# Kernel optimization log

Hardware: AMD Instinct MI355X
Metric: run time of the kernel (lower is better)

Reference implementation:

```python
import jax, jax.numpy as jnp
import numpy as np

# Static problem sizes (see shape_source)
B, D, H, W = 2, 16, 64, 64          # batch, sparse_shape = grid_size[::-1]
NV = 20000                           # active voxels per batch sample
CIN = 16                             # input_channels
THRESH = 0.5                         # FOCAL_THRESHOLD (used for kernel-offset mask)
EPS = 1e-3                           # BatchNorm eps from norm_fn
K_FORE = int(NV * THRESH)            # topk split: top int(N*threshold) voxels are foreground
# kernel_offsets: [[i,j,k] for i,j,k in (-1..1)^3] minus [0,0,0], applied to [z,y,x]
OFFSETS = [(i, j, k) for i in range(-1, 2) for j in range(-1, 2) for k in range(-1, 2) if (i, j, k) != (0, 0, 0)]


def _conv(x, w):
    # dense 3x3x3 conv == SubMConv3d math at active sites (inactive cells hold zeros)
    return jax.lax.conv_general_dilated(x, w, (1, 1, 1), 'SAME',
                                        dimension_numbers=('NDHWC', 'DHWIO', 'NDHWC'))


def _bn(x, g, b, m, v):
    # eval-mode BatchNorm1d over voxel features
    return (x - m) * (g * jax.lax.rsqrt(v + EPS)) + b


def setup_inputs() -> dict:
    rng = np.random.default_rng(0)
    coords = []
    for b in range(B):  # unique voxel coords per sample (spconv requires unique indices)
        lin = rng.permutation(D * H * W)[:NV]
        z = lin // (H * W); r = lin % (H * W)
        coords.append(np.stack([np.full(NV, b), z, r // W, r % W], 1))
    voxel_coords = jnp.asarray(np.concatenate(coords, 0), jnp.int32)  # [B*NV, 4] = [b,z,y,x]
    ks = jax.random.split(jax.random.key(0), 24)

    def bn_p(i, c):
        return (1.0 + 0.1 * jax.random.normal(ks[i], (c,)),
                0.1 * jax.random.normal(ks[i + 1], (c,)),
                0.1 * jax.random.normal(ks[i + 2], (c,)),
                jax.random.uniform(ks[i + 3], (c,), minval=0.5, maxval=1.5))

    g1, b1, m1, v1 = bn_p(4, 32)
    g2, b2, m2, v2 = bn_p(8, 64)
    g3, b3, m3, v3 = bn_p(12, 128)
    return dict(
        voxel_features=jax.random.normal(ks[0], (B * NV, CIN), jnp.float32),
        voxel_coords=voxel_coords,
        w1=0.08 * jax.random.normal(ks[1], (3, 3, 3, CIN, 32), jnp.float32),
        w2=0.06 * jax.random.normal(ks[2], (3, 3, 3, 32, 64), jnp.float32),
        w_imp=0.05 * jax.random.normal(ks[3], (3, 3, 3, 64, 27), jnp.float32),
        w_focal=0.04 * jax.random.normal(ks[16], (3, 3, 3, 64, 128), jnp.float32),
        g1=g1, b1=b1, m1=m1, v1=v1,
        g2=g2, b2=b2, m2=m2, v2=v2,
        g3=g3, b3=b3, m3=m3, v3=v3)


def reference(voxel_features, w1, g1, b1, m1, v1, w2, g2, b2, m2, v2,
              w_imp, w_focal, g3, b3, m3, v3, voxel_coords):
    bi, z, y, x = (voxel_coords[:, i] for i in range(4))
    # scatter sparse voxels into dense grid; zeros at inactive cells
    dense = jnp.zeros((B, D, H, W, CIN), voxel_features.dtype).at[bi, z, y, x].set(voxel_features)
    active = jnp.zeros((B, D, H, W), bool).at[bi, z, y, x].set(True)
    am = active[..., None].astype(voxel_features.dtype)

    # conv_input: two SubMConv3d + BN + ReLU (re-mask so inactive cells stay zero)
    h = jax.nn.relu(_bn(_conv(dense, w1), g1, b1, m1, v1)) * am   # -> 32
    h = jax.nn.relu(_bn(_conv(h, w2), g2, b2, m2, v2)) * am       # -> 64

    # conv_imp -> 27 logits; last = voxel importance, first 26 = kernel-offset importances
    imp = _conv(h, w_imp)
    mask_voxel = jax.nn.sigmoid(imp[..., -1])
    mask_kernel = jax.nn.sigmoid(imp[..., :26])

    # split_voxels with topk=True: foreground = top int(NV*thr) voxels per batch by importance
    mv_flat = jnp.where(active, mask_voxel, -jnp.inf).reshape(B, -1)
    kth = jax.lax.top_k(mv_flat, K_FORE)[0][:, -1]
    fore = active & (mask_voxel >= kth[:, None, None, None])

    # dilate foreground by kernel offsets where offset importance >= threshold.
    # New voxels carry zero features; check_repeat (index_add dedup) then reduces to:
    # final features == original features, final actives == active OR dilated candidates.
    new_act = active
    for i, (oz, oy, ox) in enumerate(OFFSETS):
        src = fore & (mask_kernel[..., i] >= THRESH)
        p = jnp.pad(src, ((0, 0), (1, 1), (1, 1), (1, 1)))  # zero(False)-pad for shift
        sh = p[:, 1 - oz:1 - oz + D, 1 - oy:1 - oy + H, 1 - ox:1 - ox + W]
        # original bound check is strict (>0), so plane 0 of each axis is invalid
        sh = sh.at[:, 0].set(False).at[:, :, 0].set(False).at[:, :, :, 0].set(False)
        new_act = new_act | sh

    # conv_focal on merged sparse set (new voxels have zero features -> dense conv matches)
    out = jax.nn.relu(_bn(_conv(h, w_focal), g3, b3, m3, v3)) * new_act[..., None].astype(h.dtype)
    return out  # densified encoded_spconv_tensor features [B, D, H, W, 128]
```

## Files before the change

kernel.cpp:

```cpp
#include <hip/hip_runtime.h>
#include <stdint.h>

#define Dd 16
#define Hh 64
#define Ww 64
#define NACT 40000
#define NVb 20000
#define KFORE 10000
#define EPSf 0.001f

typedef __attribute__((ext_vector_type(8))) short short8;
typedef __attribute__((ext_vector_type(4))) float f32x4;
typedef __attribute__((ext_vector_type(4))) unsigned short us4;

static __device__ __forceinline__ uint32_t f2sort(float f) {
    uint32_t u = __float_as_uint(f);
    return (u & 0x80000000u) ? ~u : (u | 0x80000000u);
}

static __device__ __forceinline__ unsigned short f2b(float f) {
    uint32_t u = __float_as_uint(f);
    return (unsigned short)((u + 0x7FFFu + ((u >> 16) & 1u)) >> 16);
}

static __device__ __forceinline__ int xcd_swz(int orig, int nwg) {
    int xcd = orig & 7, idx = orig >> 3;
    int q = nwg >> 3, r = nwg & 7;
    int base = xcd < r ? xcd * (q + 1) : r * (q + 1) + (xcd - r) * q;
    return base + idx;
}

__global__ void __launch_bounds__(256) k_scatter(const float* __restrict__ feat,
                                                 const int* __restrict__ coords,
                                                 float* __restrict__ dense16,
                                                 uint8_t* __restrict__ active,
                                                 uint8_t* __restrict__ new_act) {
    int i = blockIdx.x * 256 + threadIdx.x;
    if (i >= NACT) return;
    int b = coords[i * 4 + 0], z = coords[i * 4 + 1], y = coords[i * 4 + 2], x = coords[i * 4 + 3];
    int pos = ((b * Dd + z) * Hh + y) * Ww + x;
    active[pos] = 1;
    new_act[pos] = 1;
    const float4* f4 = (const float4*)(feat + (size_t)i * 16);
    float4* d4 = (float4*)(dense16 + (size_t)pos * 16);
    d4[0] = f4[0]; d4[1] = f4[1]; d4[2] = f4[2]; d4[3] = f4[3];
}

__global__ void __launch_bounds__(256) k_cnt(const uint8_t* __restrict__ mask,
                                             int* __restrict__ bcnt) {
    __shared__ int s[256];
    const int i = blockIdx.x * 256 + threadIdx.x;
    s[threadIdx.x] = mask[i] ? 1 : 0;
    __syncthreads();
    for (int off = 128; off > 0; off >>= 1) {
        if (threadIdx.x < off) s[threadIdx.x] += s[threadIdx.x + off];
        __syncthreads();
    }
    if (threadIdx.x == 0) bcnt[blockIdx.x] = s[0];
}

__global__ void __launch_bounds__(512) k_scan(const int* __restrict__ bcnt,
                                              int* __restrict__ boff, int* __restrict__ count) {
    __shared__ int s[512];
    const int t = threadIdx.x;
    const int v0 = bcnt[t];
    s[t] = v0;
    __syncthreads();
    for (int off = 1; off < 512; off <<= 1) {
        int v = s[t];
        if (t >= off) v += s[t - off];
        __syncthreads();
        s[t] = v;
        __syncthreads();
    }
    boff[t] = s[t] - v0;
    if (t == 511) *count = s[511];
}

__global__ void __launch_bounds__(256) k_emit(const uint8_t* __restrict__ mask,
                                              const int* __restrict__ boff,
                                              int* __restrict__ list) {
    __shared__ int s[256];
    const int i = blockIdx.x * 256 + threadIdx.x;
    const int pred = mask[i] ? 1 : 0;
    s[threadIdx.x] = pred;
    __syncthreads();
    for (int off = 1; off < 256; off <<= 1) {
        int v = s[threadIdx.x];
        if (threadIdx.x >= off) v += s[threadIdx.x - off];
        __syncthreads();
        s[threadIdx.x] = v;
        __syncthreads();
    }
    if (pred) list[boff[blockIdx.x] + s[threadIdx.x] - 1] = i;
}

__global__ void __launch_bounds__(256) k_conv1p(const int* __restrict__ list,
        const float* __restrict__ dense16, const float* __restrict__ w1,
        float* __restrict__ pbuf) {
    const int gb = xcd_swz(blockIdx.x, 157 * 3);
    const int chunk = gb / 3, tp = gb % 3;
    const int i = chunk * 256 + threadIdx.x;
    if (i >= NACT) return;
    const int pos = list[i];
    const int z = (pos >> 12) & 15, y = (pos >> 6) & 63, x = pos & 63;
    float acc[32];
    #pragma unroll
    for (int c = 0; c < 32; ++c) acc[c] = 0.f;
    const int dz = tp - 1;
    if ((unsigned)(z + dz) < Dd) {
        for (int tt = 0; tt < 9; ++tt) {
            const int dy = tt / 3 - 1, dx = tt % 3 - 1;
            if (!((unsigned)(y + dy) < Hh && (unsigned)(x + dx) < Ww)) continue;
            const float* row = dense16 + (size_t)(pos + dz * 4096 + dy * 64 + dx) * 16;
            const float* wt = w1 + (tp * 9 + tt) * 512;
            #pragma unroll
            for (int k4 = 0; k4 < 4; ++k4) {
                float4 xv = *(const float4*)(row + k4 * 4);
                float xs[4] = {xv.x, xv.y, xv.z, xv.w};
                #pragma unroll
                for (int j = 0; j < 4; ++j)
                    #pragma unroll
                    for (int c = 0; c < 32; ++c)
                        acc[c] = fmaf(xs[j], wt[(k4 * 4 + j) * 32 + c], acc[c]);
            }
        }
    }
    #pragma unroll
    for (int c = 0; c < 32; ++c) pbuf[(size_t)(tp * 32 + c) * NACT + i] = acc[c];
}

__global__ void __launch_bounds__(256) k_conv1c(const int* __restrict__ list,
        const float* __restrict__ pbuf,
        const float* __restrict__ g, const float* __restrict__ bta,
        const float* __restrict__ mu, const float* __restrict__ va,
        float* __restrict__ h1) {
    const int i = blockIdx.x * 256 + threadIdx.x;
    if (i >= NACT) return;
    const int pos = list[i];
    float res[32];
    #pragma unroll
    for (int c = 0; c < 32; ++c) {
        float s = pbuf[(size_t)c * NACT + i]
                + pbuf[(size_t)(32 + c) * NACT + i]
                + pbuf[(size_t)(64 + c) * NACT + i];
        const float sc = g[c] * (1.0f / sqrtf(va[c] + EPSf));
        res[c] = fmaxf(0.f, fmaf(s - mu[c], sc, bta[c]));
    }
    #pragma unroll
    for (int c4 = 0; c4 < 8; ++c4)
        *(float4*)(h1 + (size_t)pos * 32 + c4 * 4) = *(float4*)&res[c4 * 4];
}

__global__ void __launch_bounds__(256) k_conv2p(const int* __restrict__ list,
        const float* __restrict__ h1, const float* __restrict__ w2,
        float* __restrict__ pbuf) {
    const int gb = xcd_swz(blockIdx.x, 157 * 6);
    const int chunk = gb / 6, p = gb % 6;
    const int tp = p >> 1, cb = (p & 1) * 32;
    const int i = chunk * 256 + threadIdx.x;
    if (i >= NACT) return;
    const int pos = list[i];
    const int z = (pos >> 12) & 15, y = (pos >> 6) & 63, x = pos & 63;
    float acc[32];
    #pragma unroll
    for (int c = 0; c < 32; ++c) acc[c] = 0.f;
    const int dz = tp - 1;
    if ((unsigned)(z + dz) < Dd) {
        for (int tt = 0; tt < 9; ++tt) {
            const int dy = tt / 3 - 1, dx = tt % 3 - 1;
            if (!((unsigned)(y + dy) < Hh && (unsigned)(x + dx) < Ww)) continue;
            const float* row = h1 + (size_t)(pos + dz * 4096 + dy * 64 + dx) * 32;
            const float* wt = w2 + (tp * 9 + tt) * 2048 + cb;
            #pragma unroll
            for (int k4 = 0; k4 < 8; ++k4) {
                float4 xv = *(const float4*)(row + k4 * 4);
                float xs[4] = {xv.x, xv.y, xv.z, xv.w};
                #pragma unroll
                for (int j = 0; j < 4; ++j)
                    #pragma unroll
                    for (int c = 0; c < 32; ++c)
                        acc[c] = fmaf(xs[j], wt[(k4 * 4 + j) * 64 + c], acc[c]);
            }
        }
    }
    #pragma unroll
    for (int c = 0; c < 32; ++c) pbuf[(size_t)(tp * 64 + cb + c) * NACT + i] = acc[c];
}

__global__ void __launch_bounds__(256) k_conv2c(const int* __restrict__ list,
        const float* __restrict__ pbuf,
        const float* __restrict__ g, const float* __restrict__ bta,
        const float* __restrict__ mu, const float* __restrict__ va,
        float* __restrict__ h2, unsigned short* __restrict__ h2b) {
    const int i = blockIdx.x * 256 + threadIdx.x;
    if (i >= NACT) return;
    const int pos = list[i];
    float res[64];
    #pragma unroll
    for (int c = 0; c < 64; ++c) {
        float s = pbuf[(size_t)c * NACT + i]
                + pbuf[(size_t)(64 + c) * NACT + i]
                + pbuf[(size_t)(128 + c) * NACT + i];
        const float sc = g[c] * (1.0f / sqrtf(va[c] + EPSf));
        res[c] = fmaxf(0.f, fmaf(s - mu[c], sc, bta[c]));
    }
    #pragma unroll
    for (int c4 = 0; c4 < 16; ++c4)
        *(float4*)(h2 + (size_t)pos * 64 + c4 * 4) = *(float4*)&res[c4 * 4];
    #pragma unroll
    for (int c4 = 0; c4 < 16; ++c4) {
        us4 o = { f2b(res[c4 * 4]), f2b(res[c4 * 4 + 1]), f2b(res[c4 * 4 + 2]), f2b(res[c4 * 4 + 3]) };
        *(us4*)(h2b + (size_t)pos * 64 + c4 * 4) = o;
    }
}

__global__ void __launch_bounds__(256) k_impp(const int* __restrict__ list,
        const float* __restrict__ h2, const float* __restrict__ wimp,
        float* __restrict__ pbuf) {
    const int gb = xcd_swz(blockIdx.x, 157 * 9);
    const int chunk = gb / 9, tp = gb % 9;
    const int i = chunk * 256 + threadIdx.x;
    if (i >= NACT) return;
    const int pos = list[i];
    const int z = (pos >> 12) & 15, y = (pos >> 6) & 63, x = pos & 63;
    float acc[27];
    #pragma unroll
    for (int c = 0; c < 27; ++c) acc[c] = 0.f;
    for (int tt = 0; tt < 3; ++tt) {
        const int t = tp * 3 + tt;
        const int dz = t / 9 - 1, dy = (t / 3) % 3 - 1, dx = t % 3 - 1;
        if (!((unsigned)(z + dz) < Dd && (unsigned)(y + dy) < Hh && (unsigned)(x + dx) < Ww)) continue;
        const float* row = h2 + (size_t)(pos + dz * 4096 + dy * 64 + dx) * 64;
        const float* wt = wimp + t * 1728;
        #pragma unroll
        for (int k4 = 0; k4 < 16; ++k4) {
            float4 xv = *(const float4*)(row + k4 * 4);
            float xs[4] = {xv.x, xv.y, xv.z, xv.w};
            #pragma unroll
            for (int j = 0; j < 4; ++j)
                #pragma unroll
                for (int c = 0; c < 27; ++c)
                    acc[c] = fmaf(xs[j], wt[(k4 * 4 + j) * 27 + c], acc[c]);
        }
    }
    #pragma unroll
    for (int c = 0; c < 27; ++c) pbuf[(size_t)(tp * 27 + c) * NACT + i] = acc[c];
}

__global__ void __launch_bounds__(256) k_impc(const float* __restrict__ pbuf,
        uint32_t* __restrict__ u_logits, uint32_t* __restrict__ kbits) {
    const int i = blockIdx.x * 256 + threadIdx.x;
    if (i >= NACT) return;
    uint32_t bits = 0;
    float logit = 0.f;
    #pragma unroll
    for (int c = 0; c < 27; ++c) {
        float s = 0.f;
        #pragma unroll
        for (int tp = 0; tp < 9; ++tp)
            s += pbuf[(size_t)(tp * 27 + c) * NACT + i];
        if (c < 26) bits |= (s >= 0.f ? 1u : 0u) << c;
        else logit = s;
    }
    kbits[i] = bits;
    u_logits[i] = f2sort(logit);
}

__global__ void __launch_bounds__(256) k_select(const uint32_t* __restrict__ u_all,
                                                uint32_t* __restrict__ kth_u) {
    const int b = blockIdx.x;
    const uint32_t* u = u_all + (size_t)b * NVb;
    __shared__ int hist[256];
    __shared__ int s_d, s_above;
    uint32_t prefix = 0;
    int K = KFORE;
    for (int p = 3; p >= 0; --p) {
        hist[threadIdx.x] = 0;
        __syncthreads();
        const int sh = p * 8;
        for (int i = threadIdx.x; i < NVb; i += 256) {
            uint32_t ui = u[i];
            bool cand;
            if (p == 3) cand = true;
            else cand = ((ui >> (sh + 8)) == prefix);
            if (cand) atomicAdd(&hist[(ui >> sh) & 255], 1);
        }
        __syncthreads();
        if (threadIdx.x == 0) {
            int cum = 0, d = 255;
            for (; d >= 0; --d) { cum += hist[d]; if (cum >= K) break; }
            s_d = d; s_above = cum - hist[d];
        }
        __syncthreads();
        prefix = (prefix << 8) | (uint32_t)s_d;
        K -= s_above;
        __syncthreads();
    }
    if (threadIdx.x == 0) kth_u[b] = prefix;
}

__global__ void __launch_bounds__(256) k_dilate(const int* __restrict__ list,
                                                const uint32_t* __restrict__ u_logits,
                                                const uint32_t* __restrict__ kbits,
                                                const uint32_t* __restrict__ kth_u,
                                                uint8_t* __restrict__ new_act) {
    int i = blockIdx.x * 256 + threadIdx.x;
    if (i >= NACT) return;
    int pos = list[i];
    int b = pos >> 16;
    if (u_logits[i] < kth_u[b]) return;
    int z = (pos >> 12) & 15, y = (pos >> 6) & 63, x = pos & 63;
    uint32_t bits = kbits[i];
    while (bits) {
        int ch = __ffs(bits) - 1;
        bits &= bits - 1;
        int l = ch + (ch >= 13 ? 1 : 0);
        int oz = l / 9 - 1, oy = (l / 3) % 3 - 1, ox = l % 3 - 1;
        int tz = z + oz, ty = y + oy, tx = x + ox;
        if (tz >= 1 && tz < Dd && ty >= 1 && ty < Hh && tx >= 1 && tx < Ww)
            new_act[((b * Dd + tz) * Hh + ty) * Ww + tx] = 1;
    }
}

__global__ void __launch_bounds__(256) k_wcvt(const float* __restrict__ wf,
                                              unsigned short* __restrict__ wfb) {
    int i = blockIdx.x * 256 + threadIdx.x;
    int t = i >> 13, r = i & 8191, n = r >> 6, k = r & 63;
    wfb[i] = f2b(wf[(t * 64 + k) * 128 + n]);
}

__global__ void __launch_bounds__(256, 4) k_focal(
        const int* __restrict__ list, const int* __restrict__ count,
        const unsigned short* __restrict__ h2b, const unsigned short* __restrict__ wfb,
        const float* __restrict__ g, const float* __restrict__ bta,
        const float* __restrict__ mu, const float* __restrict__ va,
        float* __restrict__ out, const unsigned short* __restrict__ zb) {
    __shared__ __align__(16) unsigned short As[2][64 * 64];
    __shared__ int s_pos[64];
    const int n = *count;
    const int i0 = xcd_swz(blockIdx.x, 2048) * 64;
    if (i0 >= n) return;
    const int tid = threadIdx.x;
    const int wv = tid >> 6, lane = tid & 63;
    if (tid < 64) { int idx = i0 + tid; s_pos[tid] = idx < n ? list[idx] : -1; }
    __syncthreads();
    const int v0 = tid >> 3, c8 = tid & 7, v1 = v0 + 32;
    const int p0 = s_pos[v0], p1 = s_pos[v1];
    const int z0 = (p0 >> 12) & 15, y0 = (p0 >> 6) & 63, x0 = p0 & 63;
    const int z1 = (p1 >> 12) & 15, y1 = (p1 >> 6) & 63, x1 = p1 & 63;
    const int wslot = (c8 ^ (v0 & 7)) << 3;
    const int wa0 = v0 * 64 + wslot, wa1 = v1 * 64 + wslot;
    const int hi = lane >> 4, lo = lane & 15;
    const int cb = wv * 32;

    f32x4 acc[4][2];
    #pragma unroll
    for (int mi = 0; mi < 4; ++mi)
        #pragma unroll
        for (int ni = 0; ni < 2; ++ni) acc[mi][ni] = (f32x4){0.f, 0.f, 0.f, 0.f};

    auto stage_src = [&](int t, const unsigned short*& a0, const unsigned short*& a1) {
        int dz = t / 9 - 1, dy = (t / 3) % 3 - 1, dx = t % 3 - 1;
        int off = dz * 4096 + dy * 64 + dx;
        bool ok0 = p0 >= 0 && (unsigned)(z0 + dz) < Dd && (unsigned)(y0 + dy) < Hh && (unsigned)(x0 + dx) < Ww;
        bool ok1 = p1 >= 0 && (unsigned)(z1 + dz) < Dd && (unsigned)(y1 + dy) < Hh && (unsigned)(x1 + dx) < Ww;
        a0 = ok0 ? h2b + (size_t)(p0 + off) * 64 + c8 * 8 : zb;
        a1 = ok1 ? h2b + (size_t)(p1 + off) * 64 + c8 * 8 : zb;
    };

    {
        const unsigned short *a0p, *a1p;
        stage_src(0, a0p, a1p);
        *(short8*)&As[0][wa0] = *(const short8*)a0p;
        *(short8*)&As[0][wa1] = *(const short8*)a1p;
    }
    __syncthreads();

    for (int t = 0; t < 27; ++t) {
        const int cur = t & 1;
        short8 r0, r1;
        if (t < 26) {
            const unsigned short *a0p, *a1p;
            stage_src(t + 1, a0p, a1p);
            r0 = *(const short8*)a0p;
            r1 = *(const short8*)a1p;
        }
        short8 bfr[2][2];
        #pragma unroll
        for (int ni = 0; ni < 2; ++ni)
            #pragma unroll
            for (int ks = 0; ks < 2; ++ks)
                bfr[ni][ks] = *(const short8*)(wfb + (size_t)t * 8192
                                + (size_t)(cb + ni * 16 + lo) * 64 + ks * 32 + hi * 8);
        #pragma unroll
        for (int ks = 0; ks < 2; ++ks) {
            const int rs = ((ks * 4 + hi) ^ (lo & 7)) << 3;
            short8 a[4];
            #pragma unroll
            for (int mi = 0; mi < 4; ++mi)
                a[mi] = *(const short8*)&As[cur][(mi * 16 + lo) * 64 + rs];
            #pragma unroll
            for (int mi = 0; mi < 4; ++mi)
                #pragma unroll
                for (int ni = 0; ni < 2; ++ni)
                    acc[mi][ni] = __builtin_amdgcn_mfma_f32_16x16x32_bf16(
                        a[mi], bfr[ni][ks], acc[mi][ni], 0, 0, 0);
        }
        if (t < 26) {
            *(short8*)&As[1 - cur][wa0] = r0;
            *(short8*)&As[1 - cur][wa1] = r1;
            __syncthreads();
        }
    }

    #pragma unroll
    for (int ni = 0; ni < 2; ++ni) {
        const int ch = cb + ni * 16 + lo;
        const float s = g[ch] * (1.0f / sqrtf(va[ch] + EPSf));
        const float sh = bta[ch], mm = mu[ch];
        #pragma unroll
        for (int mi = 0; mi < 4; ++mi)
            #pragma unroll
            for (int j = 0; j < 4; ++j) {
                int vi = mi * 16 + hi * 4 + j;
                if (i0 + vi < n)
                    out[(size_t)s_pos[vi] * 128 + ch] = fmaxf(0.f, fmaf(acc[mi][ni][j] - mm, s, sh));
            }
    }
}

extern "C" void kernel_launch(void* const* d_in, const int* in_sizes, int n_in,
                              void* d_out, int out_size, void* d_ws, size_t ws_size,
                              hipStream_t stream) {
    (void)in_sizes; (void)n_in; (void)ws_size;
    const float* feat   = (const float*)d_in[0];
    const int*   coords = (const int*)d_in[1];
    const float* w1   = (const float*)d_in[2];
    const float* w2   = (const float*)d_in[3];
    const float* wimp = (const float*)d_in[4];
    const float* wf   = (const float*)d_in[5];
    const float* g1 = (const float*)d_in[6],  *b1 = (const float*)d_in[7];
    const float* m1 = (const float*)d_in[8],  *v1 = (const float*)d_in[9];
    const float* g2 = (const float*)d_in[10], *b2 = (const float*)d_in[11];
    const float* m2 = (const float*)d_in[12], *v2 = (const float*)d_in[13];
    const float* g3 = (const float*)d_in[14], *b3 = (const float*)d_in[15];
    const float* m3 = (const float*)d_in[16], *v3 = (const float*)d_in[17];

    char* ws = (char*)d_ws;
    float*    dense16  = (float*)(ws + 0);
    float*    h1       = (float*)(ws + 8388608);
    float*    h2       = (float*)(ws + 25165824);
    uint8_t*  active   = (uint8_t*)(ws + 58720256);
    uint8_t*  new_act  = (uint8_t*)(ws + 58851328);
    float*    zrow     = (float*)(ws + 58982400);
    int*      count    = (int*)(ws + 58982656);
    const size_t MEMSET_BYTES = 58982912;
    uint32_t* u_logits = (uint32_t*)(ws + 58982912);
    uint32_t* kbits    = (uint32_t*)(ws + 59142912);
    uint32_t* kth_u    = (uint32_t*)(ws + 59302912);
    int*      list     = (int*)(ws + 59303168);

    unsigned short* wfb = (unsigned short*)dense16;
    unsigned short* h2b = (unsigned short*)h1;
    float* pbuf = (float*)d_out;
    int* bcnt = (int*)kbits;
    int* boff = (int*)kbits + 512;

    hipMemsetAsync(d_ws, 0, MEMSET_BYTES, stream);

    k_scatter<<<157, 256, 0, stream>>>(feat, coords, dense16, active, new_act);
    k_cnt<<<512, 256, 0, stream>>>(active, bcnt);
    k_scan<<<1, 512, 0, stream>>>(bcnt, boff, count);
    k_emit<<<512, 256, 0, stream>>>(active, boff, list);
    k_conv1p<<<157 * 3, 256, 0, stream>>>(list, dense16, w1, pbuf);
    k_conv1c<<<157, 256, 0, stream>>>(list, pbuf, g1, b1, m1, v1, h1);
    k_wcvt<<<864, 256, 0, stream>>>(wf, wfb);
    k_conv2p<<<157 * 6, 256, 0, stream>>>(list, h1, w2, pbuf);
    hipMemsetAsync(h2b, 0, (size_t)131072 * 64 * 2, stream);
    k_conv2c<<<157, 256, 0, stream>>>(list, pbuf, g2, b2, m2, v2, h2, h2b);
    k_impp<<<157 * 9, 256, 0, stream>>>(list, h2, wimp, pbuf);
    k_impc<<<157, 256, 0, stream>>>(pbuf, u_logits, kbits);
    hipMemsetAsync(d_out, 0, (size_t)out_size * sizeof(float), stream);
    k_select<<<2, 256, 0, stream>>>(u_logits, kth_u);
    k_dilate<<<157, 256, 0, stream>>>(list, u_logits, kbits, kth_u, new_act);
    k_cnt<<<512, 256, 0, stream>>>(new_act, bcnt);
    k_scan<<<1, 512, 0, stream>>>(bcnt, boff, count);
    k_emit<<<512, 256, 0, stream>>>(new_act, boff, list);
    k_focal<<<2048, 256, 0, stream>>>(list, count, h2b, wfb, g3, b3, m3, v3,
                                      (float*)d_out, (const unsigned short*)zrow);
}
```

Before: 583.1 us.

## Merge conv2 channel halves per thread and deepen focal-conv gather prefetch

k_conv2p now has each thread compute all 64 output channels for its z-tap instead of splitting them into two 32-channel blocks. This halves the grid and the redundant gathers of h1 neighbour rows, at the cost of 64 accumulator registers per thread. In k_focal the double-buffered loop is restructured so neighbour rows are gathered two taps ahead into registers, putting more latency between each global load and its use in the MFMA step. That adds register pressure and more involved buffer indexing.

```diff
diff --git a/kernel.cpp b/kernel.cpp
--- a/kernel.cpp
+++ b/kernel.cpp
@@ -155,23 +155,22 @@
 __global__ void __launch_bounds__(256) k_conv2p(const int* __restrict__ list,
         const float* __restrict__ h1, const float* __restrict__ w2,
         float* __restrict__ pbuf) {
-    const int gb = xcd_swz(blockIdx.x, 157 * 6);
-    const int chunk = gb / 6, p = gb % 6;
-    const int tp = p >> 1, cb = (p & 1) * 32;
+    const int gb = xcd_swz(blockIdx.x, 157 * 3);
+    const int chunk = gb / 3, tp = gb % 3;
     const int i = chunk * 256 + threadIdx.x;
     if (i >= NACT) return;
     const int pos = list[i];
     const int z = (pos >> 12) & 15, y = (pos >> 6) & 63, x = pos & 63;
-    float acc[32];
-    #pragma unroll
-    for (int c = 0; c < 32; ++c) acc[c] = 0.f;
+    float acc[64];
+    #pragma unroll
+    for (int c = 0; c < 64; ++c) acc[c] = 0.f;
     const int dz = tp - 1;
     if ((unsigned)(z + dz) < Dd) {
         for (int tt = 0; tt < 9; ++tt) {
             const int dy = tt / 3 - 1, dx = tt % 3 - 1;
             if (!((unsigned)(y + dy) < Hh && (unsigned)(x + dx) < Ww)) continue;
             const float* row = h1 + (size_t)(pos + dz * 4096 + dy * 64 + dx) * 32;
-            const float* wt = w2 + (tp * 9 + tt) * 2048 + cb;
+            const float* wt = w2 + (tp * 9 + tt) * 2048;
             #pragma unroll
             for (int k4 = 0; k4 < 8; ++k4) {
                 float4 xv = *(const float4*)(row + k4 * 4);
@@ -179,13 +178,13 @@
                 #pragma unroll
                 for (int j = 0; j < 4; ++j)
                     #pragma unroll
-                    for (int c = 0; c < 32; ++c)
+                    for (int c = 0; c < 64; ++c)
                         acc[c] = fmaf(xs[j], wt[(k4 * 4 + j) * 64 + c], acc[c]);
             }
         }
     }
     #pragma unroll
-    for (int c = 0; c < 32; ++c) pbuf[(size_t)(tp * 64 + cb + c) * NACT + i] = acc[c];
+    for (int c = 0; c < 64; ++c) pbuf[(size_t)(tp * 64 + c) * NACT + i] = acc[c];
 }
 
 __global__ void __launch_bounds__(256) k_conv2c(const int* __restrict__ list,
@@ -360,32 +359,16 @@
         #pragma unroll
         for (int ni = 0; ni < 2; ++ni) acc[mi][ni] = (f32x4){0.f, 0.f, 0.f, 0.f};
 
-    auto stage_src = [&](int t, const unsigned short*& a0, const unsigned short*& a1) {
+    auto gather = [&](int t, short8& r0, short8& r1) {
         int dz = t / 9 - 1, dy = (t / 3) % 3 - 1, dx = t % 3 - 1;
         int off = dz * 4096 + dy * 64 + dx;
         bool ok0 = p0 >= 0 && (unsigned)(z0 + dz) < Dd && (unsigned)(y0 + dy) < Hh && (unsigned)(x0 + dx) < Ww;
         bool ok1 = p1 >= 0 && (unsigned)(z1 + dz) < Dd && (unsigned)(y1 + dy) < Hh && (unsigned)(x1 + dx) < Ww;
-        a0 = ok0 ? h2b + (size_t)(p0 + off) * 64 + c8 * 8 : zb;
-        a1 = ok1 ? h2b + (size_t)(p1 + off) * 64 + c8 * 8 : zb;
+        r0 = *(const short8*)(ok0 ? h2b + (size_t)(p0 + off) * 64 + c8 * 8 : zb);
+        r1 = *(const short8*)(ok1 ? h2b + (size_t)(p1 + off) * 64 + c8 * 8 : zb);
     };
 
-    {
-        const unsigned short *a0p, *a1p;
-        stage_src(0, a0p, a1p);
-        *(short8*)&As[0][wa0] = *(const short8*)a0p;
-        *(short8*)&As[0][wa1] = *(const short8*)a1p;
-    }
-    __syncthreads();
-
-    for (int t = 0; t < 27; ++t) {
-        const int cur = t & 1;
-        short8 r0, r1;
-        if (t < 26) {
-            const unsigned short *a0p, *a1p;
-            stage_src(t + 1, a0p, a1p);
-            r0 = *(const short8*)a0p;
-            r1 = *(const short8*)a1p;
-        }
+    auto compute = [&](int t, int buf) {
         short8 bfr[2][2];
         #pragma unroll
         for (int ni = 0; ni < 2; ++ni)
@@ -399,7 +382,7 @@
             short8 a[4];
             #pragma unroll
             for (int mi = 0; mi < 4; ++mi)
-                a[mi] = *(const short8*)&As[cur][(mi * 16 + lo) * 64 + rs];
+                a[mi] = *(const short8*)&As[buf][(mi * 16 + lo) * 64 + rs];
             #pragma unroll
             for (int mi = 0; mi < 4; ++mi)
                 #pragma unroll
@@ -407,12 +390,36 @@
                     acc[mi][ni] = __builtin_amdgcn_mfma_f32_16x16x32_bf16(
                         a[mi], bfr[ni][ks], acc[mi][ni], 0, 0, 0);
         }
-        if (t < 26) {
-            *(short8*)&As[1 - cur][wa0] = r0;
-            *(short8*)&As[1 - cur][wa1] = r1;
-            __syncthreads();
-        }
-    }
+    };
+
+    short8 rA0, rA1, rB0, rB1;
+    gather(0, rA0, rA1);
+    gather(1, rB0, rB1);
+    *(short8*)&As[0][wa0] = rA0; *(short8*)&As[0][wa1] = rA1;
+    *(short8*)&As[1][wa0] = rB0; *(short8*)&As[1][wa1] = rB1;
+    gather(2, rA0, rA1);
+    gather(3, rB0, rB1);
+    __syncthreads();
+
+    for (int t = 0; t < 26; t += 2) {
+        compute(t, 0);
+        __syncthreads();
+        if (t + 2 <= 26) {
+            *(short8*)&As[0][wa0] = rA0;
+            *(short8*)&As[0][wa1] = rA1;
+            if (t + 4 <= 26) gather(t + 4, rA0, rA1);
+        }
+        compute(t + 1, 1);
+        __syncthreads();
+        if (t + 3 <= 26) {
+            *(short8*)&As[1][wa0] = rB0;
+            *(short8*)&As[1][wa1] = rB1;
+            if (t + 5 <= 26) gather(t + 5, rB0, rB1);
+        }
+        if (t + 2 > 26) break;
+    }
+    __syncthreads();
+    compute(26, 0);
 
     #pragma unroll
     for (int ni = 0; ni < 2; ++ni) {
@@ -476,7 +483,7 @@
     k_conv1p<<<157 * 3, 256, 0, stream>>>(list, dense16, w1, pbuf);
     k_conv1c<<<157, 256, 0, stream>>>(list, pbuf, g1, b1, m1, v1, h1);
     k_wcvt<<<864, 256, 0, stream>>>(wf, wfb);
-    k_conv2p<<<157 * 6, 256, 0, stream>>>(list, h1, w2, pbuf);
+    k_conv2p<<<157 * 3, 256, 0, stream>>>(list, h1, w2, pbuf);
     hipMemsetAsync(h2b, 0, (size_t)131072 * 64 * 2, stream);
     k_conv2c<<<157, 256, 0, stream>>>(list, pbuf, g2, b2, m2, v2, h2, h2b);
     k_impp<<<157 * 9, 256, 0, stream>>>(list, h2, wimp, pbuf);
```

Result: slower. 646.2 us (+10.8%).
